# Performance work log

Hardware: AMD Instinct MI355X
Metric: run time of the kernel (lower is better)

Reference implementation:

```python
import jax, jax.numpy as jnp
import numpy as np

B, H, W, C = 8, 112, 112, 192
NH = 6
HD = C // NH
WS = 7            # window size
SS = 3            # shift size (WS//2)
N = WS * WS       # tokens per window (49)
NW = (H // WS) * (W // WS)  # windows per image
EPS = 1e-5
LOG100 = float(np.log(100.0))


def _rel_bias_consts():
    # continuous relative coords table, shape ((2*WS-1)^2, 2), log-spaced
    r = np.arange(-(WS - 1), WS, dtype=np.float32)
    table = np.stack(np.meshgrid(r, r, indexing='ij')).transpose(1, 2, 0).reshape(-1, 2)
    table = table / float(max(WS - 1, 1)) * 8.0
    table = np.sign(table) * np.log2(np.abs(table) + 1.0) / np.log2(8.0)
    # relative position index, shape (N*N,)
    coords = np.stack(np.meshgrid(np.arange(WS), np.arange(WS), indexing='ij')).reshape(2, -1)
    rel = (coords[:, :, None] - coords[:, None, :]).transpose(1, 2, 0) + (WS - 1)
    idx = (rel * np.array([2 * WS - 1, 1])).sum(-1).astype(np.int32).reshape(-1)
    return jnp.asarray(table), jnp.asarray(idx)


def _shift_attn_mask():
    # standard Swin shifted-window attention mask, shape (NW, N, N)
    img = np.zeros((H, W), np.float32)
    cnt = 0
    for hs in (slice(0, -WS), slice(-WS, -SS), slice(-SS, None)):
        for ws_ in (slice(0, -WS), slice(-WS, -SS), slice(-SS, None)):
            img[hs, ws_] = cnt
            cnt += 1
    win = img.reshape(H // WS, WS, W // WS, WS).transpose(0, 2, 1, 3).reshape(-1, N)
    diff = win[:, None, :] - win[:, :, None]
    return jnp.asarray(np.where(diff != 0, -100.0, 0.0).astype(np.float32))


_TABLE, _IDX = _rel_bias_consts()
_MASK = _shift_attn_mask()


def _ln(x, g, b):
    m = jnp.mean(x, axis=-1, keepdims=True)
    v = jnp.mean((x - m) ** 2, axis=-1, keepdims=True)
    return (x - m) / jnp.sqrt(v + EPS) * g + b


def setup_inputs() -> dict:
    key = jax.random.key(0)
    ks = jax.random.split(key, 8)
    s = 0.02
    return {
        'x': jax.random.normal(ks[0], (B, H * W, C), jnp.float32),
        'ln1_g': jnp.ones((C,), jnp.float32), 'ln1_b': jnp.zeros((C,), jnp.float32),
        'ln2_g': jnp.ones((C,), jnp.float32), 'ln2_b': jnp.zeros((C,), jnp.float32),
        'q_w': jax.random.normal(ks[1], (C, C), jnp.float32) * s,
        'q_b': jnp.zeros((C,), jnp.float32),
        'k_w': jax.random.normal(ks[2], (C, C), jnp.float32) * s,
        'v_w': jax.random.normal(ks[3], (C, C), jnp.float32) * s,
        'v_b': jnp.zeros((C,), jnp.float32),
        'p_w': jax.random.normal(ks[4], (C, C), jnp.float32) * s,
        'p_b': jnp.zeros((C,), jnp.float32),
        'logit_scale': jnp.log(10.0 * jnp.ones((NH, 1, 1), jnp.float32)),
        'cpb_w0': jax.random.normal(ks[5], (2, 512), jnp.float32) * s,
        'cpb_b0': jnp.zeros((512,), jnp.float32),
        'cpb_w1': jax.random.normal(ks[6], (512, NH), jnp.float32) * s,
        'fc1_w': jax.random.normal(ks[7], (C, 4 * C), jnp.float32) * s,
        'fc1_b': jnp.zeros((4 * C,), jnp.float32),
        'fc2_w': jax.random.normal(jax.random.fold_in(key, 9), (4 * C, C), jnp.float32) * s,
        'fc2_b': jnp.zeros((C,), jnp.float32),
    }


def reference(x, ln1_g, ln1_b, ln2_g, ln2_b, q_w, q_b, k_w, v_w, v_b, p_w, p_b,
              logit_scale, cpb_w0, cpb_b0, cpb_w1, fc1_w, fc1_b, fc2_w, fc2_b):
    shortcut = x
    h = x.reshape(B, H, W, C)
    h = jnp.roll(h, (-SS, -SS), axis=(1, 2))                       # cyclic shift
    # window partition -> (B*NW, N, C)
    win = h.reshape(B, H // WS, WS, W // WS, WS, C).transpose(0, 1, 3, 2, 4, 5)
    win = win.reshape(B * NW, N, C)

    q = (win @ q_w + q_b).reshape(-1, N, NH, HD).transpose(0, 2, 1, 3)  # (BW,h,N,d)
    k = (win @ k_w).reshape(-1, N, NH, HD).transpose(0, 2, 1, 3)
    v = (win @ v_w + v_b).reshape(-1, N, NH, HD).transpose(0, 2, 1, 3)

    # cosine attention with learned clamped logit scale
    qn = q / jnp.maximum(jnp.linalg.norm(q, axis=-1, keepdims=True), 1e-12)
    kn = k / jnp.maximum(jnp.linalg.norm(k, axis=-1, keepdims=True), 1e-12)
    scale = jnp.exp(jnp.minimum(logit_scale, LOG100))              # (h,1,1)
    attn = jnp.einsum('whqd,whkd->whqk', qn, kn) * scale

    # continuous relative position bias: MLP(2->512->h), gather, 16*sigmoid
    t = jax.nn.relu(_TABLE @ cpb_w0 + cpb_b0) @ cpb_w1             # ((2WS-1)^2, h)
    bias = t[_IDX].reshape(N, N, NH).transpose(2, 0, 1)            # (h,N,N)
    attn = attn + 16.0 * jax.nn.sigmoid(bias)[None]

    # shifted-window mask
    attn = attn.reshape(B, NW, NH, N, N) + _MASK[None, :, None]
    attn = jax.nn.softmax(attn.reshape(B * NW, NH, N, N), axis=-1)

    out = jnp.einsum('whqk,whkd->whqd', attn, v)                   # (BW,h,N,d)
    out = out.transpose(0, 2, 1, 3).reshape(B * NW, N, C)
    out = out @ p_w + p_b

    # window reverse + un-shift
    out = out.reshape(B, H // WS, W // WS, WS, WS, C).transpose(0, 1, 3, 2, 4, 5)
    out = out.reshape(B, H, W, C)
    out = jnp.roll(out, (SS, SS), axis=(1, 2)).reshape(B, H * W, C)

    # swin-v2 res-post-norm residuals
    hidden = shortcut + _ln(out, ln1_g, ln1_b)
    mlp = jax.nn.gelu(hidden @ fc1_w + fc1_b) @ fc2_w + fc2_b
    return hidden + _ln(mlp, ln2_g, ln2_b)
```

## Files before the change

### kernel.cpp

```cpp
#include <hip/hip_runtime.h>


typedef __bf16  bf16x8 __attribute__((ext_vector_type(8)));
typedef float   f32x4  __attribute__((ext_vector_type(4)));

__device__ __forceinline__ float bf2f(unsigned short u){
    return __uint_as_float(((unsigned int)u) << 16);
}
__device__ __forceinline__ unsigned short f2bf(float f){
    unsigned int u = __float_as_uint(f);
    unsigned int r = (u + 0x7fffu + ((u >> 16) & 1u)) >> 16;
    return (unsigned short)r;
}
__device__ __forceinline__ float ldin(const void* p, size_t i, int f32){
    return f32 ? ((const float*)p)[i] : bf2f(((const unsigned short*)p)[i]);
}
__device__ __forceinline__ void gl_lds16(const unsigned short* g, unsigned short* l){
    __builtin_amdgcn_global_load_lds(
        (const __attribute__((address_space(1))) unsigned int*)g,
        (__attribute__((address_space(3))) unsigned int*)l, 16, 0, 0);
}

__global__ void detect_kernel(const unsigned short* __restrict__ ln1g, int* __restrict__ flag){
    if (threadIdx.x == 0) *flag = (ln1g[0] == 0x3F80u) ? 0 : 1;
}

__global__ __launch_bounds__(256)
void pack_kernel(const void* __restrict__ qw, const void* __restrict__ kw,
                 const void* __restrict__ vw, const void* __restrict__ qb,
                 const void* __restrict__ vb, const void* __restrict__ pw,
                 const void* __restrict__ pb, const void* __restrict__ f1w,
                 const void* __restrict__ f1b, const void* __restrict__ f2w,
                 const void* __restrict__ f2b,
                 const void* __restrict__ l1g, const void* __restrict__ l1b,
                 const void* __restrict__ l2g, const void* __restrict__ l2b,
                 unsigned short* __restrict__ wqkvt, unsigned short* __restrict__ pwt,
                 unsigned short* __restrict__ f1t, unsigned short* __restrict__ f2t,
                 float* __restrict__ qkv_bias, float* __restrict__ p_bias,
                 float* __restrict__ f1_bias, float* __restrict__ f2_bias,
                 float* __restrict__ lnp, const int* __restrict__ dtf)
{
    int f32 = *dtf;
    int i = blockIdx.x * 256 + threadIdx.x;
    if (i < 110592){
        int n = i / 192, k = i - n * 192;
        float s = (n < 192) ? ldin(qw, (size_t)k*192 + n, f32)
                 : (n < 384) ? ldin(kw, (size_t)k*192 + (n-192), f32)
                 : ldin(vw, (size_t)k*192 + (n-384), f32);
        wqkvt[n*192 + k] = f2bf(s);
    }
    if (i < 36864){
        int n = i / 192, k = i - n * 192;
        pwt[n*192 + k] = f2bf(ldin(pw, (size_t)k*192 + n, f32));
    }
    if (i < 147456){
        int n = i / 192, k = i - n * 192;
        f1t[n*192 + k] = f2bf(ldin(f1w, (size_t)k*768 + n, f32));
        int n2 = i / 768, k2 = i - n2 * 768;
        f2t[n2*768 + k2] = f2bf(ldin(f2w, (size_t)k2*192 + n2, f32));
    }
    if (i < 576) qkv_bias[i] = (i < 192) ? ldin(qb, i, f32)
                              : (i < 384) ? 0.f : ldin(vb, i-384, f32);
    if (i < 192){
        p_bias[i]  = ldin(pb, i, f32);
        f2_bias[i] = ldin(f2b, i, f32);
        lnp[i]       = ldin(l1g, i, f32);
        lnp[192+i]   = ldin(l1b, i, f32);
        lnp[384+i]   = ldin(l2g, i, f32);
        lnp[576+i]   = ldin(l2b, i, f32);
    }
    if (i < 768) f1_bias[i] = ldin(f1b, i, f32);
}

__device__ __forceinline__ float cpb_coord(int a){
    float v = (float)(a - 6) * (8.0f / 6.0f);
    float s = (v > 0.f) ? 1.f : (v < 0.f ? -1.f : 0.f);
    return s * log2f(fabsf(v) + 1.f) * (1.f / 3.f);
}

__global__ __launch_bounds__(256)
void cpb_kernel(const void* __restrict__ ls, const void* __restrict__ w0,
                const void* __restrict__ b0, const void* __restrict__ w1,
                float* __restrict__ bmask, float* __restrict__ scale,
                const int* __restrict__ dtf)
{
    __shared__ float w0a[512], w0b[512], b0s[512], w1s[512];
    __shared__ float tv[169];
    __shared__ float sval[2401];
    int f32 = *dtf;
    int tid = threadIdx.x;
    int h = blockIdx.x;

    for (int c = tid; c < 512; c += 256){
        w0a[c] = ldin(w0, c, f32);
        w0b[c] = ldin(w0, 512 + c, f32);
        b0s[c] = ldin(b0, c, f32);
        w1s[c] = ldin(w1, (size_t)c*6 + h, f32);
    }
    __syncthreads();

    for (int q = tid; q < 169; q += 256){
        int a = q / 13, b = q - a * 13;
        float t0 = cpb_coord(a), t1 = cpb_coord(b);
        float acc = 0.f;
        for (int c = 0; c < 512; ++c){
            float hv = fmaxf(t0 * w0a[c] + t1 * w0b[c] + b0s[c], 0.f);
            acc += hv * w1s[c];
        }
        tv[q] = acc;
    }
    __syncthreads();

    for (int e = tid; e < 2401; e += 256){
        int i = e / 49, j = e - i * 49;
        int di = i/7 - j/7 + 6;
        int dj = (i - (i/7)*7) - (j - (j/7)*7) + 6;
        sval[e] = 16.f / (1.f + expf(-tv[di*13 + dj]));
    }
    __syncthreads();

    for (int t = 0; t < 4; ++t){
        int ey = t >> 1, ex = t & 1;
        for (int e = tid; e < 4096; e += 256){
            int row = e >> 6, li = e & 63;
            int lrow = li >> 2, f = li & 3;
            int col = f*16 + lrow;
            float val;
            if (row >= 49) val = 0.f;
            else if (col >= 49) val = -1e30f;
            else {
                val = sval[row*49 + col];
                int rr = row/7, rc = row - rr*7;
                int cr = col/7, cc = col - cr*7;
                int ridr = (ey ? (rr < 4 ? 1 : 2) : 0)*3 + (ex ? (rc < 4 ? 1 : 2) : 0);
                int ridc = (ey ? (cr < 4 ? 1 : 2) : 0)*3 + (ex ? (cc < 4 ? 1 : 2) : 0);
                if (ridr != ridc) val -= 100.f;
            }
            bmask[(((size_t)(h*4 + t)*64 + row) << 6) + li] = val;
        }
    }
    if (tid == 0) scale[h] = expf(fminf(ldin(ls, h, f32), 4.6051702f));
}

template<int GATHER, int EPI>
__device__ __forceinline__ size_t gemm_aoff(int t, int K){
    if (GATHER){
        int w = t / 49, p = t - w * 49;
        int bb = w >> 8, widx = w & 255;
        int wy = widx >> 4, wx = widx & 15;
        int r = p / 7, c = p - r * 7;
        int oy = (wy*7 + r + 3) % 112;
        int ox = (wx*7 + c + 3) % 112;
        return ((size_t)bb * 12544 + (size_t)oy * 112 + ox) * 192;
    }
    return (size_t)t * K;
}

template<int GATHER, int EPI>
__global__ __launch_bounds__(256)
void gemm_kernel(const void* __restrict__ A,
                 const unsigned short* __restrict__ Bt,
                 const float* __restrict__ bias,
                 unsigned short* __restrict__ Cout,
                 int M, int N, int K, const int* __restrict__ dtf)
{
    __shared__ unsigned short As[2][128][32];
    __shared__ unsigned short Bs[2][192][32];

    int f32 = GATHER ? *dtf : 0;
    int tid = threadIdx.x;
    int nb = N / 192;
    int bng = blockIdx.x % nb;
    int bm  = (blockIdx.x / nb) * 128;
    int bn0 = bng * 192;

    int wv = tid >> 6, ln = tid & 63;
    int lrow4 = ln >> 2, lseg = ln & 3;

    const unsigned short* Ag0; const unsigned short* Ag1;
    {
        int r0 = bm + wv*32 + lrow4;
        Ag0 = (const unsigned short*)A + gemm_aoff<GATHER,EPI>(r0, K) + lseg*8;
        Ag1 = (const unsigned short*)A + gemm_aoff<GATHER,EPI>(r0 + 16, K) + lseg*8;
    }
    const unsigned short* Bg = Bt + (size_t)(bn0 + wv*48 + lrow4) * K + lseg*8;
    size_t bstep = (size_t)16 * K;

    int wm = wv * 32;
    int quad = ln >> 4, lrow = ln & 15;

    f32x4 acc[12][2] = {};

    if (GATHER && f32){
        int arow = tid >> 2, aseg = tid & 3;
        size_t aoff0 = gemm_aoff<GATHER,EPI>(bm + arow, K);
        size_t aoff1 = gemm_aoff<GATHER,EPI>(bm + arow + 64, K);
        const unsigned short* brp0 = Bt + (size_t)(bn0       + arow) * K;
        const unsigned short* brp1 = Bt + (size_t)(bn0 +  64 + arow) * K;
        const unsigned short* brp2 = Bt + (size_t)(bn0 + 128 + arow) * K;
        for (int k0 = 0; k0 < K; k0 += 32){
            __syncthreads();
            const float* p0 = (const float*)A + aoff0 + k0 + aseg*8;
            const float* p1 = (const float*)A + aoff1 + k0 + aseg*8;
            unsigned short t8[8];
            #pragma unroll
            for (int j = 0; j < 8; ++j) t8[j] = f2bf(p0[j]);
            *(uint4*)(&As[0][arow][aseg*8]) = *(const uint4*)t8;
            #pragma unroll
            for (int j = 0; j < 8; ++j) t8[j] = f2bf(p1[j]);
            *(uint4*)(&As[0][arow + 64][aseg*8]) = *(const uint4*)t8;
            *(uint4*)(&Bs[0][arow      ][aseg*8]) = *(const uint4*)(brp0 + k0 + aseg*8);
            *(uint4*)(&Bs[0][arow +  64][aseg*8]) = *(const uint4*)(brp1 + k0 + aseg*8);
            *(uint4*)(&Bs[0][arow + 128][aseg*8]) = *(const uint4*)(brp2 + k0 + aseg*8);
            __syncthreads();
            bf16x8 a0 = *(const bf16x8*)(&As[0][wm      + lrow][quad*8]);
            bf16x8 a1 = *(const bf16x8*)(&As[0][wm + 16 + lrow][quad*8]);
            #pragma unroll
            for (int f = 0; f < 12; ++f){
                bf16x8 bb = *(const bf16x8*)(&Bs[0][f*16 + lrow][quad*8]);
                acc[f][0] = __builtin_amdgcn_mfma_f32_16x16x32_bf16(a0, bb, acc[f][0], 0, 0, 0);
                acc[f][1] = __builtin_amdgcn_mfma_f32_16x16x32_bf16(a1, bb, acc[f][1], 0, 0, 0);
            }
        }
    } else {
        gl_lds16(Ag0,                 &As[0][wv*32     ][0]);
        gl_lds16(Ag1,                 &As[0][wv*32 + 16][0]);
        gl_lds16(Bg,                  &Bs[0][wv*48     ][0]);
        gl_lds16(Bg + bstep,          &Bs[0][wv*48 + 16][0]);
        gl_lds16(Bg + 2*bstep,        &Bs[0][wv*48 + 32][0]);
        int cur = 0;
        for (int k0 = 0; k0 < K; k0 += 32){
            asm volatile("s_waitcnt vmcnt(0)" ::: "memory");
            __builtin_amdgcn_s_barrier();
            __builtin_amdgcn_sched_barrier(0);
            if (k0 + 32 < K){
                int nk = k0 + 32, nb_ = cur ^ 1;
                gl_lds16(Ag0 + nk,            &As[nb_][wv*32     ][0]);
                gl_lds16(Ag1 + nk,            &As[nb_][wv*32 + 16][0]);
                gl_lds16(Bg  + nk,            &Bs[nb_][wv*48     ][0]);
                gl_lds16(Bg  + bstep + nk,    &Bs[nb_][wv*48 + 16][0]);
                gl_lds16(Bg  + 2*bstep + nk,  &Bs[nb_][wv*48 + 32][0]);
            }
            bf16x8 a0 = *(const bf16x8*)(&As[cur][wm      + lrow][quad*8]);
            bf16x8 a1 = *(const bf16x8*)(&As[cur][wm + 16 + lrow][quad*8]);
            #pragma unroll
            for (int f = 0; f < 12; ++f){
                bf16x8 bb = *(const bf16x8*)(&Bs[cur][f*16 + lrow][quad*8]);
                acc[f][0] = __builtin_amdgcn_mfma_f32_16x16x32_bf16(a0, bb, acc[f][0], 0, 0, 0);
                acc[f][1] = __builtin_amdgcn_mfma_f32_16x16x32_bf16(a1, bb, acc[f][1], 0, 0, 0);
            }
            cur ^= 1;
        }
    }

    #pragma unroll
    for (int f = 0; f < 12; ++f)
    #pragma unroll
    for (int tm = 0; tm < 2; ++tm)
    #pragma unroll
    for (int i = 0; i < 4; ++i){
        int row = bm + wm + tm*16 + quad*4 + i;
        int col = bn0 + f*16 + lrow;
        float v = acc[f][tm][i] + bias[col];
        if (EPI == 1){
            float t = __expf(v * fmaf(v*v, -0.071354816f, -1.5957691216f));
            v = v * __builtin_amdgcn_rcpf(1.f + t);
        }
        Cout[(size_t)row * N + col] = f2bf(v);
    }
}

__global__ __launch_bounds__(256)
void attn_kernel(const unsigned short* __restrict__ qkv,
                 const float* __restrict__ bmask,
                 const float* __restrict__ scale,
                 unsigned short* __restrict__ attn_out)
{
    __shared__ unsigned short qb[64][40];
    __shared__ unsigned short kb[64][40];
    __shared__ unsigned short vT[32][72];
    __shared__ unsigned short Ps[64][72];
    __shared__ float rnq[64], rnk[64];

    int tid = threadIdx.x;
    int w = blockIdx.x, h = blockIdx.y;
    int widx = w & 255;
    int wy = widx >> 4, wx = widx & 15;
    int mtype = ((wy == 15) ? 2 : 0) | ((wx == 15) ? 1 : 0);

    size_t wbase = (size_t)w * 49 * 576 + (size_t)h * 32;

    for (int e = tid; e < 512; e += 256){
        int p = e >> 3, s = e & 7;
        uint2 zq = {0u, 0u}, zk = {0u, 0u};
        if (p < 49){
            size_t g = wbase + (size_t)p * 576 + s * 4;
            zq = *(const uint2*)&qkv[g];
            zk = *(const uint2*)&qkv[g + 192];
        }
        *(uint2*)&qb[p][s*4] = zq;
        *(uint2*)&kb[p][s*4] = zk;
    }
    for (int e = tid; e < 2048; e += 256){
        int p = e >> 5, d = e & 31;
        vT[d][p] = (p < 49) ? qkv[wbase + (size_t)p * 576 + 384 + d]
                            : (unsigned short)0;
    }
    __syncthreads();

    {
        int row = tid >> 2, seg = tid & 3;
        bf16x8 qv = *(const bf16x8*)&qb[row][seg * 8];
        bf16x8 kv = *(const bf16x8*)&kb[row][seg * 8];
        float q2 = 0.f, k2 = 0.f;
        #pragma unroll
        for (int j = 0; j < 8; ++j){
            float a = (float)qv[j], b = (float)kv[j];
            q2 = fmaf(a, a, q2);
            k2 = fmaf(b, b, k2);
        }
        q2 += __shfl_xor(q2, 1);  q2 += __shfl_xor(q2, 2);
        k2 += __shfl_xor(k2, 1);  k2 += __shfl_xor(k2, 2);
        if (seg == 0){
            rnq[row] = scale[h] * rsqrtf(fmaxf(q2, 1e-24f));
            rnk[row] = rsqrtf(fmaxf(k2, 1e-24f));
        }
    }
    __syncthreads();

    int wave = tid >> 6, lane = tid & 63;
    int quad = lane >> 4, lrow = lane & 15;
    int wm = wave * 16;

    bf16x8 aq = *(const bf16x8*)&qb[wm + lrow][quad * 8];
    f32x4 sfr[4];
    #pragma unroll
    for (int f = 0; f < 4; ++f){
        bf16x8 bk = *(const bf16x8*)&kb[f*16 + lrow][quad * 8];
        f32x4 z = {0.f, 0.f, 0.f, 0.f};
        sfr[f] = __builtin_amdgcn_mfma_f32_16x16x32_bf16(aq, bk, z, 0, 0, 0);
    }

    float rk[4];
    #pragma unroll
    for (int f = 0; f < 4; ++f) rk[f] = rnk[f*16 + lrow];
    const float4* bmp = (const float4*)bmask + (size_t)(h*4 + mtype) * 1024;
    #pragma unroll
    for (int reg = 0; reg < 4; ++reg){
        int row = wm + quad*4 + reg;
        float rq = rnq[row];
        float4 bm = bmp[row*16 + lrow];
        float v0 = fmaf(sfr[0][reg], rq*rk[0], bm.x);
        float v1 = fmaf(sfr[1][reg], rq*rk[1], bm.y);
        float v2 = fmaf(sfr[2][reg], rq*rk[2], bm.z);
        float v3 = fmaf(sfr[3][reg], rq*rk[3], bm.w);
        float mx = fmaxf(fmaxf(v0, v1), fmaxf(v2, v3));
        #pragma unroll
        for (int m = 8; m; m >>= 1) mx = fmaxf(mx, __shfl_xor(mx, m));
        float e0 = __expf(v0 - mx), e1 = __expf(v1 - mx);
        float e2 = __expf(v2 - mx), e3 = __expf(v3 - mx);
        float sm = (e0 + e1) + (e2 + e3);
        #pragma unroll
        for (int m = 8; m; m >>= 1) sm += __shfl_xor(sm, m);
        float inv = 1.f / sm;
        Ps[row][ 0 + lrow] = f2bf(e0 * inv);
        Ps[row][16 + lrow] = f2bf(e1 * inv);
        Ps[row][32 + lrow] = f2bf(e2 * inv);
        Ps[row][48 + lrow] = f2bf(e3 * inv);
    }
    __syncthreads();

    f32x4 o[2] = {{0.f,0.f,0.f,0.f}, {0.f,0.f,0.f,0.f}};
    #pragma unroll
    for (int c = 0; c < 2; ++c){
        bf16x8 ap = *(const bf16x8*)&Ps[wm + lrow][c*32 + quad*8];
        #pragma unroll
        for (int n = 0; n < 2; ++n){
            bf16x8 bv = *(const bf16x8*)&vT[n*16 + lrow][c*32 + quad*8];
            o[n] = __builtin_amdgcn_mfma_f32_16x16x32_bf16(ap, bv, o[n], 0, 0, 0);
        }
    }
    __syncthreads();

    unsigned short (*Os)[40] = qb;
    #pragma unroll
    for (int n = 0; n < 2; ++n)
    #pragma unroll
    for (int reg = 0; reg < 4; ++reg){
        int row = wm + quad*4 + reg;
        if (row < 49) Os[row][n*16 + lrow] = f2bf(o[n][reg]);
    }
    __syncthreads();

    for (int e = tid; e < 392; e += 256){
        int p = e >> 3, c4 = (e & 7) * 4;
        uint2 val = *(const uint2*)&Os[p][c4];
        *(uint2*)&attn_out[((size_t)w*49 + p)*192 + (size_t)h*32 + c4] = val;
    }
}

template<int FINAL>
__global__ __launch_bounds__(256)
void ln_kernel(const void* __restrict__ base,
               const unsigned short* __restrict__ src,
               const float* __restrict__ g,
               const float* __restrict__ b,
               void* __restrict__ dst, const int* __restrict__ dtf)
{
    int f32 = *dtf;
    int tid = threadIdx.x;
    int lane = tid & 63;
    int token = blockIdx.x * 4 + (tid >> 6);

    size_t srow;
    if (FINAL){
        srow = (size_t)token * 192;
    } else {
        int bb = token / 12544, pix = token - bb*12544;
        int y = pix / 112, x = pix - y*112;
        int gy = (y + 109) % 112, gx = (x + 109) % 112;
        int wy = gy / 7, r = gy - wy*7;
        int wx = gx / 7, c = gx - wx*7;
        int t = (bb*256 + wy*16 + wx)*49 + r*7 + c;
        srow = (size_t)t * 192;
    }

    float o[3]; float s = 0.f;
    #pragma unroll
    for (int j = 0; j < 3; ++j){ o[j] = bf2f(src[srow + j*64 + lane]); s += o[j]; }
    #pragma unroll
    for (int off = 32; off; off >>= 1) s += __shfl_xor(s, off);
    float m = s * (1.f/192.f);
    float vsum = 0.f;
    #pragma unroll
    for (int j = 0; j < 3; ++j){ float d = o[j] - m; vsum += d*d; }
    #pragma unroll
    for (int off = 32; off; off >>= 1) vsum += __shfl_xor(vsum, off);
    float rstd = rsqrtf(vsum * (1.f/192.f) + 1e-5f);

    size_t brow = (size_t)token * 192;
    #pragma unroll
    for (int j = 0; j < 3; ++j){
        int cidx = j*64 + lane;
        float bv = FINAL ? bf2f(((const unsigned short*)base)[brow + cidx])
                         : ldin(base, brow + cidx, f32);
        float val = bv + (o[j] - m) * rstd * g[cidx] + b[cidx];
        if (FINAL){
            if (f32) ((float*)dst)[brow + cidx] = val;
            else     ((unsigned short*)dst)[brow + cidx] = f2bf(val);
        } else {
            ((unsigned short*)dst)[brow + cidx] = f2bf(val);
        }
    }
}

extern "C" void kernel_launch(void* const* d_in, const int* in_sizes, int n_in,
                              void* d_out, int out_size, void* d_ws, size_t ws_size,
                              hipStream_t stream)
{
    const void* x    = d_in[0];
    const void* ln1g = d_in[1];
    const void* ln1b = d_in[2];
    const void* ln2g = d_in[3];
    const void* ln2b = d_in[4];
    const void* qw   = d_in[5];
    const void* qb   = d_in[6];
    const void* kw   = d_in[7];
    const void* vw   = d_in[8];
    const void* vb   = d_in[9];
    const void* pw   = d_in[10];
    const void* pb   = d_in[11];
    const void* ls   = d_in[12];
    const void* w0   = d_in[13];
    const void* b0   = d_in[14];
    const void* w1   = d_in[15];
    const void* f1w  = d_in[16];
    const void* f1b  = d_in[17];
    const void* f2w  = d_in[18];
    const void* f2b  = d_in[19];

    char* ws = (char*)d_ws;
    unsigned short* big    = (unsigned short*)(ws);
    unsigned short* bufB   = (unsigned short*)(ws + 154140672);
    unsigned short* hidden = (unsigned short*)(ws + 192675840);
    unsigned short* wqkvt  = (unsigned short*)(ws + 231211008);
    unsigned short* pwt    = (unsigned short*)(ws + 231211008 + 221184);
    unsigned short* f1t    = (unsigned short*)(ws + 231211008 + 221184 + 73728);
    unsigned short* f2t    = (unsigned short*)(ws + 231211008 + 221184 + 73728 + 294912);
    float* qkv_bias = (float*)(ws + 232095744);
    float* p_bias   = qkv_bias + 576;
    float* f1_bias  = p_bias + 192;
    float* f2_bias  = f1_bias + 768;
    float* bmask    = (float*)(ws + 232102656);
    float* scale    = (float*)(ws + 232495872);
    float* lnp      = (float*)(ws + 232495896);
    int*   dtf      = (int*)  (ws + 232498968);

    detect_kernel<<<1, 64, 0, stream>>>((const unsigned short*)ln1g, dtf);
    pack_kernel<<<576, 256, 0, stream>>>(qw, kw, vw, qb, vb, pw, pb, f1w, f1b, f2w, f2b,
                                         ln1g, ln1b, ln2g, ln2b,
                                         wqkvt, pwt, f1t, f2t,
                                         qkv_bias, p_bias, f1_bias, f2_bias, lnp, dtf);
    cpb_kernel<<<6, 256, 0, stream>>>(ls, w0, b0, w1, bmask, scale, dtf);

    gemm_kernel<1,0><<<784*3, 256, 0, stream>>>(x, wqkvt, qkv_bias, big, 100352, 576, 192, dtf);
    attn_kernel<<<dim3(2048, 6), 256, 0, stream>>>(big, bmask, scale, bufB);
    gemm_kernel<0,0><<<784, 256, 0, stream>>>(bufB, pwt, p_bias, big, 100352, 192, 192, dtf);
    ln_kernel<0><<<25088, 256, 0, stream>>>(x, big, lnp, lnp + 192, hidden, dtf);
    gemm_kernel<0,1><<<784*4, 256, 0, stream>>>(hidden, f1t, f1_bias, big, 100352, 768, 192, dtf);
    gemm_kernel<0,0><<<784, 256, 0, stream>>>(big, f2t, f2_bias, bufB, 100352, 192, 768, dtf);
    ln_kernel<1><<<25088, 256, 0, stream>>>(hidden, bufB, lnp + 384, lnp + 576, d_out, dtf);

    (void)in_sizes; (void)n_in; (void)out_size; (void)ws_size;
}
```

Baseline: 535.7 us.

## Fuse post-norm LayerNorm and residual into projection and fc2 GEMM epilogues

After: 576.7 us. 7.7% more time.

```diff
diff --git a/kernel.cpp b/kernel.cpp
--- a/kernel.cpp
+++ b/kernel.cpp
@@ -162,12 +162,15 @@
                  const unsigned short* __restrict__ Bt,
                  const float* __restrict__ bias,
                  unsigned short* __restrict__ Cout,
-                 int M, int N, int K, const int* __restrict__ dtf)
+                 int M, int N, int K, const int* __restrict__ dtf,
+                 const float* __restrict__ lng, const float* __restrict__ lnb,
+                 const void* __restrict__ basep)
 {
     __shared__ unsigned short As[2][128][32];
     __shared__ unsigned short Bs[2][192][32];
 
     int f32 = GATHER ? *dtf : 0;
+    int f32out = (EPI >= 2) ? *dtf : 0;
     int tid = threadIdx.x;
     int nb = N / 192;
     int bng = blockIdx.x % nb;
@@ -253,20 +256,56 @@
         }
     }
 
-    #pragma unroll
-    for (int f = 0; f < 12; ++f)
-    #pragma unroll
-    for (int tm = 0; tm < 2; ++tm)
-    #pragma unroll
-    for (int i = 0; i < 4; ++i){
-        int row = bm + wm + tm*16 + quad*4 + i;
-        int col = bn0 + f*16 + lrow;
-        float v = acc[f][tm][i] + bias[col];
-        if (EPI == 1){
-            float t = __expf(v * fmaf(v*v, -0.071354816f, -1.5957691216f));
-            v = v * __builtin_amdgcn_rcpf(1.f + t);
-        }
-        Cout[(size_t)row * N + col] = f2bf(v);
+    if (EPI >= 2){
+        #pragma unroll
+        for (int tm = 0; tm < 2; ++tm)
+        #pragma unroll
+        for (int i = 0; i < 4; ++i){
+            int row = bm + wm + tm*16 + quad*4 + i;
+            float v[12]; float s = 0.f, q = 0.f;
+            #pragma unroll
+            for (int f = 0; f < 12; ++f){
+                v[f] = acc[f][tm][i] + bias[f*16 + lrow];
+                s += v[f]; q = fmaf(v[f], v[f], q);
+            }
+            #pragma unroll
+            for (int m_ = 1; m_ < 16; m_ <<= 1){
+                s += __shfl_xor(s, m_);
+                q += __shfl_xor(q, m_);
+            }
+            float mean = s * (1.f/192.f);
+            float rstd = rsqrtf(fmaxf(q * (1.f/192.f) - mean*mean, 0.f) + 1e-5f);
+            size_t obase = (EPI == 2) ? gemm_aoff<1,EPI>(row, 192) : (size_t)row * 192;
+            #pragma unroll
+            for (int f = 0; f < 12; ++f){
+                int col = f*16 + lrow;
+                float bv = (EPI == 2) ? ldin(basep, obase + col, f32out)
+                                      : bf2f(((const unsigned short*)basep)[obase + col]);
+                float val = bv + (v[f] - mean) * rstd * lng[col] + lnb[col];
+                if (EPI == 2){
+                    Cout[obase + col] = f2bf(val);
+                } else {
+                    if (f32out) ((float*)Cout)[obase + col] = val;
+                    else        Cout[obase + col] = f2bf(val);
+                }
+            }
+        }
+    } else {
+        #pragma unroll
+        for (int f = 0; f < 12; ++f)
+        #pragma unroll
+        for (int tm = 0; tm < 2; ++tm)
+        #pragma unroll
+        for (int i = 0; i < 4; ++i){
+            int row = bm + wm + tm*16 + quad*4 + i;
+            int col = bn0 + f*16 + lrow;
+            float v = acc[f][tm][i] + bias[col];
+            if (EPI == 1){
+                float t = __expf(v * fmaf(v*v, -0.071354816f, -1.5957691216f));
+                v = v * __builtin_amdgcn_rcpf(1.f + t);
+            }
+            Cout[(size_t)row * N + col] = f2bf(v);
+        }
     }
 }
 
@@ -396,61 +435,6 @@
         int p = e >> 3, c4 = (e & 7) * 4;
         uint2 val = *(const uint2*)&Os[p][c4];
         *(uint2*)&attn_out[((size_t)w*49 + p)*192 + (size_t)h*32 + c4] = val;
-    }
-}
-
-template<int FINAL>
-__global__ __launch_bounds__(256)
-void ln_kernel(const void* __restrict__ base,
-               const unsigned short* __restrict__ src,
-               const float* __restrict__ g,
-               const float* __restrict__ b,
-               void* __restrict__ dst, const int* __restrict__ dtf)
-{
-    int f32 = *dtf;
-    int tid = threadIdx.x;
-    int lane = tid & 63;
-    int token = blockIdx.x * 4 + (tid >> 6);
-
-    size_t srow;
-    if (FINAL){
-        srow = (size_t)token * 192;
-    } else {
-        int bb = token / 12544, pix = token - bb*12544;
-        int y = pix / 112, x = pix - y*112;
-        int gy = (y + 109) % 112, gx = (x + 109) % 112;
-        int wy = gy / 7, r = gy - wy*7;
-        int wx = gx / 7, c = gx - wx*7;
-        int t = (bb*256 + wy*16 + wx)*49 + r*7 + c;
-        srow = (size_t)t * 192;
-    }
-
-    float o[3]; float s = 0.f;
-    #pragma unroll
-    for (int j = 0; j < 3; ++j){ o[j] = bf2f(src[srow + j*64 + lane]); s += o[j]; }
-    #pragma unroll
-    for (int off = 32; off; off >>= 1) s += __shfl_xor(s, off);
-    float m = s * (1.f/192.f);
-    float vsum = 0.f;
-    #pragma unroll
-    for (int j = 0; j < 3; ++j){ float d = o[j] - m; vsum += d*d; }
-    #pragma unroll
-    for (int off = 32; off; off >>= 1) vsum += __shfl_xor(vsum, off);
-    float rstd = rsqrtf(vsum * (1.f/192.f) + 1e-5f);
-
-    size_t brow = (size_t)token * 192;
-    #pragma unroll
-    for (int j = 0; j < 3; ++j){
-        int cidx = j*64 + lane;
-        float bv = FINAL ? bf2f(((const unsigned short*)base)[brow + cidx])
-                         : ldin(base, brow + cidx, f32);
-        float val = bv + (o[j] - m) * rstd * g[cidx] + b[cidx];
-        if (FINAL){
-            if (f32) ((float*)dst)[brow + cidx] = val;
-            else     ((unsigned short*)dst)[brow + cidx] = f2bf(val);
-        } else {
-            ((unsigned short*)dst)[brow + cidx] = f2bf(val);
-        }
     }
 }
 
@@ -503,13 +487,16 @@
                                          qkv_bias, p_bias, f1_bias, f2_bias, lnp, dtf);
     cpb_kernel<<<6, 256, 0, stream>>>(ls, w0, b0, w1, bmask, scale, dtf);
 
-    gemm_kernel<1,0><<<784*3, 256, 0, stream>>>(x, wqkvt, qkv_bias, big, 100352, 576, 192, dtf);
+    gemm_kernel<1,0><<<784*3, 256, 0, stream>>>(x, wqkvt, qkv_bias, big, 100352, 576, 192, dtf,
+                                                nullptr, nullptr, nullptr);
     attn_kernel<<<dim3(2048, 6), 256, 0, stream>>>(big, bmask, scale, bufB);
-    gemm_kernel<0,0><<<784, 256, 0, stream>>>(bufB, pwt, p_bias, big, 100352, 192, 192, dtf);
-    ln_kernel<0><<<25088, 256, 0, stream>>>(x, big, lnp, lnp + 192, hidden, dtf);
-    gemm_kernel<0,1><<<784*4, 256, 0, stream>>>(hidden, f1t, f1_bias, big, 100352, 768, 192, dtf);
-    gemm_kernel<0,0><<<784, 256, 0, stream>>>(big, f2t, f2_bias, bufB, 100352, 192, 768, dtf);
-    ln_kernel<1><<<25088, 256, 0, stream>>>(hidden, bufB, lnp + 384, lnp + 576, d_out, dtf);
+    gemm_kernel<0,2><<<784, 256, 0, stream>>>(bufB, pwt, p_bias, hidden, 100352, 192, 192, dtf,
+                                              lnp, lnp + 192, x);
+    gemm_kernel<0,1><<<784*4, 256, 0, stream>>>(hidden, f1t, f1_bias, big, 100352, 768, 192, dtf,
+                                                nullptr, nullptr, nullptr);
+    gemm_kernel<0,3><<<784, 256, 0, stream>>>(big, f2t, f2_bias, (unsigned short*)d_out,
+                                              100352, 192, 768, dtf,
+                                              lnp + 384, lnp + 576, hidden);
 
     (void)in_sizes; (void)n_in; (void)out_size; (void)ws_size;
 }
```
